# Kernel optimization log

Measured on AMD Instinct MI355X. Metric: run time of the kernel, lower is better.

## Reference

```python
import jax, jax.numpy as jnp
import numpy as np

N_NODES = 25000
N_EDGES = 400000
FEAT = 128
HID = 64
HEADS = 4
NUM_CLASSES = 2
NUM_GRAPHS = 64


def setup_inputs() -> dict:
    key = jax.random.key(0)
    ks = jax.random.split(key, 16)
    x = jax.random.normal(ks[0], (N_NODES, FEAT), dtype=jnp.float32)
    edge_index = jax.random.randint(ks[1], (2, N_EDGES), 0, N_NODES, dtype=jnp.int32)
    batch = jnp.sort(jax.random.randint(ks[2], (N_NODES,), 0, NUM_GRAPHS, dtype=jnp.int32))
    s = 1.0 / np.sqrt(FEAT)
    sh = 1.0 / np.sqrt(HID)
    shc = 1.0 / np.sqrt(HID * HEADS)
    return {
        "x": x,
        "edge_index": edge_index,
        "batch": batch,
        # conv1: GraphConv(FEAT -> HID): lin_rel (bias) on aggregated neighbors + lin_root (no bias)
        "W1_rel": jax.random.uniform(ks[3], (FEAT, HID), jnp.float32, -s, s),
        "b1": jnp.zeros((HID,), jnp.float32),
        "W1_root": jax.random.uniform(ks[4], (FEAT, HID), jnp.float32, -s, s),
        # conv3: GATConv(HID -> HID, heads=HEADS), concat output [N, HEADS*HID]
        "Wg": jax.random.uniform(ks[5], (HID, HEADS * HID), jnp.float32, -sh, sh),
        "att_src": jax.random.uniform(ks[6], (HEADS, HID), jnp.float32, -sh, sh),
        "att_dst": jax.random.uniform(ks[7], (HEADS, HID), jnp.float32, -sh, sh),
        "bg": jnp.zeros((HEADS * HID,), jnp.float32),
        # conv5: GraphConv(HEADS*HID -> HID)
        "W5_rel": jax.random.uniform(ks[8], (HEADS * HID, HID), jnp.float32, -shc, shc),
        "b5": jnp.zeros((HID,), jnp.float32),
        "W5_root": jax.random.uniform(ks[9], (HEADS * HID, HID), jnp.float32, -shc, shc),
        # fc head
        "W_fc1": jax.random.uniform(ks[10], (HID, HID), jnp.float32, -sh, sh),
        "b_fc1": jnp.zeros((HID,), jnp.float32),
        "W_fc2": jax.random.uniform(ks[11], (HID, NUM_CLASSES), jnp.float32, -sh, sh),
        "b_fc2": jnp.zeros((NUM_CLASSES,), jnp.float32),
    }


def _graph_conv(h, src, dst, W_rel, b, W_root):
    # PyG GraphConv (aggr='add'): out_i = W_rel @ sum_{j->i} h_j + b + W_root @ h_i
    agg = jax.ops.segment_sum(h[src], dst, num_segments=N_NODES)
    return agg @ W_rel + b + h @ W_root


def _gat_conv(h, src, dst, Wg, att_src, att_dst, bg):
    # GATConv with default add_self_loops=True; eval mode (no attn dropout)
    n = h.shape[0]
    loop = jnp.arange(n, dtype=src.dtype)
    si = jnp.concatenate([src, loop])
    di = jnp.concatenate([dst, loop])
    xl = (h @ Wg).reshape(n, HEADS, HID)              # [N, H, C]
    a_s = jnp.sum(xl * att_src, axis=-1)              # [N, H]
    a_d = jnp.sum(xl * att_dst, axis=-1)              # [N, H]
    e = jax.nn.leaky_relu(a_s[si] + a_d[di], 0.2)     # [E', H]
    m = jax.ops.segment_max(e, di, num_segments=n)
    p = jnp.exp(e - m[di])
    denom = jax.ops.segment_sum(p, di, num_segments=n)
    alpha = p / denom[di]                             # segment softmax over incoming edges
    out = jax.ops.segment_sum(alpha[:, :, None] * xl[si], di, num_segments=n)
    return out.reshape(n, HEADS * HID) + bg


def reference(x, edge_index, batch, W1_rel, b1, W1_root, Wg, att_src, att_dst, bg,
              W5_rel, b5, W5_root, W_fc1, b_fc1, W_fc2, b_fc2):
    src, dst = edge_index[0], edge_index[1]
    h = jax.nn.relu(_graph_conv(x, src, dst, W1_rel, b1, W1_root))
    h = jax.nn.relu(_gat_conv(h, src, dst, Wg, att_src, att_dst, bg))
    h = jax.nn.relu(_graph_conv(h, src, dst, W5_rel, b5, W5_root))
    g = jax.ops.segment_sum(h, batch, num_segments=NUM_GRAPHS)   # global_add_pool
    g = jax.nn.relu(g @ W_fc1 + b_fc1)
    return jax.nn.sigmoid(g @ W_fc2 + b_fc2)
```

## Files before the change

### kernel.cpp

```cpp
#include <hip/hip_runtime.h>
#include <math.h>

#define N_NODES 25000
#define N_EDGES 400000
#define FEAT 128
#define HID 64
#define HEADS 4
#define HH 256
#define NUM_GRAPHS 64
#define BUCKET 96
#define HS 1601536
#define NPH 25600
#define FILL_BLOCKS 1563

typedef unsigned short ushort_t;
typedef unsigned int uint_t;
typedef __attribute__((ext_vector_type(8))) short short8;
typedef __attribute__((ext_vector_type(4))) float f32x4;

__device__ __forceinline__ float lrelu(float x){ return x > 0.f ? x : 0.2f*x; }

__device__ __forceinline__ ushort_t f2bf(float f){
  uint_t u = __float_as_uint(f);
  return (ushort_t)((u + 0x7fffu + ((u >> 16) & 1u)) >> 16);
}
#define BF_LO(u) __uint_as_float((u) << 16)
#define BF_HI(u) __uint_as_float((u) & 0xffff0000u)

__global__ __launch_bounds__(256) void k_init(
    const float* __restrict__ W1_rel, const float* __restrict__ W1_root,
    const float* __restrict__ W5_rel, const float* __restrict__ W5_root,
    const float* __restrict__ Wg,
    ushort_t* __restrict__ wc1b, ushort_t* __restrict__ wc5b,
    ushort_t* __restrict__ wgb, float* __restrict__ g ,
    ushort_t* __restrict__ slot)
{
  const int e = blockIdx.x*256 + threadIdx.x;
  {
    int j=e&7, lane=(e>>3)&63, kc=(e>>9)&3, nt=e>>11;
    int k = kc*32 + (lane>>4)*8 + j, n = nt*16 + (lane&15);
    float v = (n < 64) ? W1_rel[k*64 + n] : W1_root[k*64 + n - 64];
    wc1b[e] = f2bf(v);
  }
  {
    int j=e&7, lane=(e>>3)&63, kt=(e>>9)&1, nt=e>>10;
    int k = kt*32 + (lane>>4)*8 + j, n = nt*16 + (lane&15);
    wgb[e] = f2bf(Wg[k*HH + n]);
  }
  #pragma unroll
  for (int e5 = e; e5 < 32768; e5 += 16384){
    int j=e5&7, lane=(e5>>3)&63, kc=(e5>>9)&7, nt=e5>>12;
    int k = kc*32 + (lane>>4)*8 + j, n = nt*16 + (lane&15);
    float v = (n < 64) ? W5_rel[k*64 + n] : W5_root[k*64 + n - 64];
    wc5b[e5] = f2bf(v);
  }
  int* z = (int*)g;
  for (int i = e; i < 4096 + N_NODES; i += 16384) z[i] = 0;
  const uint4 zz = {0,0,0,0};
  for (int n = e; n < N_NODES; n += 16384){
    uint4* p = (uint4*)(slot + (size_t)n*BUCKET);
    p[0] = zz; p[1] = zz; p[2] = zz; p[3] = zz;
  }
}

__global__ __launch_bounds__(256) void k_c1_fill(
    const int* __restrict__ src, const int* __restrict__ dst,
    int* __restrict__ cnt, ushort_t* __restrict__ slot,
    const float* __restrict__ X, const ushort_t* __restrict__ wc1b,
    const float* __restrict__ bias,
    ushort_t* __restrict__ out_rel_b, ushort_t* __restrict__ out_root_b)
{
  if (blockIdx.x < FILL_BLOCKS){
    const int e = blockIdx.x*256 + threadIdx.x;
    if (e < N_EDGES){
      int d = dst[e];
      int pos = atomicAdd(&cnt[d], 1);
      if (pos < BUCKET) slot[(size_t)d*BUCKET + pos] = (ushort_t)src[e];
    }
    return;
  }
  const int wid  = __builtin_amdgcn_readfirstlane(threadIdx.x >> 6);
  const int lane = threadIdx.x & 63;
  const int quad = lane >> 4, col = lane & 15;
  const int nb = (blockIdx.x - FILL_BLOCKS)*64 + wid*16;
  if (nb >= N_NODES) return;
  const int row = min(nb + col, N_NODES-1);
  const float* __restrict__ xr = X + (size_t)row*FEAT + quad*8;
  short8 a[4];
  #pragma unroll
  for (int kc = 0; kc < 4; kc++){
    #pragma unroll
    for (int j = 0; j < 8; j++)
      ((ushort_t*)&a[kc])[j] = f2bf(xr[kc*32 + j]);
  }
  #pragma unroll
  for (int nt = 0; nt < 8; nt++){
    f32x4 d = {0.f,0.f,0.f,0.f};
    #pragma unroll
    for (int kc = 0; kc < 4; kc++){
      short8 b = *(const short8*)(wc1b + ((size_t)(nt*4+kc)*64 + lane)*8);
      d = __builtin_amdgcn_mfma_f32_16x16x32_bf16(a[kc], b, d, 0, 0, 0);
    }
    if (nt < 4){
      #pragma unroll
      for (int r = 0; r < 4; r++){
        const int node = nb + quad*4 + r;
        if (node < N_NODES)
          out_rel_b[(size_t)node*HID + nt*16 + col] = f2bf(d[r]);
      }
    } else {
      const float bv = bias[(nt-4)*16 + col];
      #pragma unroll
      for (int r = 0; r < 4; r++){
        const int node = nb + quad*4 + r;
        if (node < N_NODES)
          out_root_b[(size_t)node*HID + (nt-4)*16 + col] = f2bf(d[r] + bv);
      }
    }
  }
}

__global__ __launch_bounds__(256) void conv5_mfma(
    const ushort_t* __restrict__ h2b_hm, const ushort_t* __restrict__ wc5b,
    const float* __restrict__ bias,
    ushort_t* __restrict__ out_rel_b, ushort_t* __restrict__ out_root_b)
{
  const int wid  = __builtin_amdgcn_readfirstlane(threadIdx.x >> 6);
  const int lane = threadIdx.x & 63;
  const int quad = lane >> 4, col = lane & 15;
  const int nb = blockIdx.x*64 + wid*16;
  if (nb >= N_NODES) return;
  const int row = nb + col;
  short8 a[8];
  #pragma unroll
  for (int kc = 0; kc < 8; kc++){
    const int k0 = kc*32 + quad*8;
    a[kc] = *(const short8*)(h2b_hm + (size_t)(k0>>6)*HS
                             + (size_t)row*HID + (k0&63));
  }
  #pragma unroll
  for (int nt = 0; nt < 8; nt++){
    f32x4 d = {0.f,0.f,0.f,0.f};
    #pragma unroll
    for (int kc = 0; kc < 8; kc++){
      short8 b = *(const short8*)(wc5b + ((size_t)(nt*8+kc)*64 + lane)*8);
      d = __builtin_amdgcn_mfma_f32_16x16x32_bf16(a[kc], b, d, 0, 0, 0);
    }
    if (nt < 4){
      #pragma unroll
      for (int r = 0; r < 4; r++){
        const int node = nb + quad*4 + r;
        if (node < N_NODES)
          out_rel_b[(size_t)node*HID + nt*16 + col] = f2bf(d[r]);
      }
    } else {
      const float bv = bias[(nt-4)*16 + col];
      #pragma unroll
      for (int r = 0; r < 4; r++){
        const int node = nb + quad*4 + r;
        if (node < N_NODES)
          out_root_b[(size_t)node*HID + (nt-4)*16 + col] = f2bf(d[r] + bv);
      }
    }
  }
}

__global__ __launch_bounds__(256) void k3_mfma(
    const ushort_t* __restrict__ h1b, const ushort_t* __restrict__ wgb,
    const float* __restrict__ att_src, const float* __restrict__ att_dst,
    ushort_t* __restrict__ xlb_hm, float* __restrict__ a_s_hm,
    float* __restrict__ a_d_hm)
{
  const int wid  = __builtin_amdgcn_readfirstlane(threadIdx.x >> 6);
  const int lane = threadIdx.x & 63;
  const int quad = lane >> 4, col = lane & 15;
  const int nb = blockIdx.x*64 + wid*16;
  const ushort_t* arow = h1b + (size_t)(nb + col)*HID + quad*8;
  short8 a0 = *(const short8*)(arow);
  short8 a1 = *(const short8*)(arow + 32);
  float as_acc[4] = {0,0,0,0}, ad_acc[4] = {0,0,0,0};
  #pragma unroll
  for (int nt = 0; nt < 16; nt++){
    short8 b0 = *(const short8*)(wgb + ((size_t)(nt*2+0)*64 + lane)*8);
    short8 b1 = *(const short8*)(wgb + ((size_t)(nt*2+1)*64 + lane)*8);
    f32x4 d = {0.f, 0.f, 0.f, 0.f};
    d = __builtin_amdgcn_mfma_f32_16x16x32_bf16(a0, b0, d, 0, 0, 0);
    d = __builtin_amdgcn_mfma_f32_16x16x32_bf16(a1, b1, d, 0, 0, 0);
    const int h = nt >> 2;
    const float asv = att_src[h*HID + (nt & 3)*16 + col];
    const float adv = att_dst[h*HID + (nt & 3)*16 + col];
    #pragma unroll
    for (int r = 0; r < 4; r++){
      const int node = nb + quad*4 + r;
      if (node < N_NODES)
        xlb_hm[(size_t)h*HS + (size_t)node*HID + (nt&3)*16 + col] = f2bf(d[r]);
      as_acc[r] += d[r]*asv;
      ad_acc[r] += d[r]*adv;
    }
    if ((nt & 3) == 3){
      #pragma unroll
      for (int r = 0; r < 4; r++){
        float s1 = as_acc[r], s2 = ad_acc[r];
        #pragma unroll
        for (int off = 1; off < 16; off <<= 1){
          s1 += __shfl_xor(s1, off, 64);
          s2 += __shfl_xor(s2, off, 64);
        }
        const int node = nb + quad*4 + r;
        if (col == 0 && node < N_NODES){
          a_s_hm[h*NPH + node] = s1;
          a_d_hm[h*NPH + node] = s2;
        }
        as_acc[r] = 0.f; ad_acc[r] = 0.f;
      }
    }
  }
}

template<int MODE>
__global__ __launch_bounds__(256, 8) void k_aggb(
    const int* __restrict__ cnt, const ushort_t* __restrict__ slot,
    const ushort_t* __restrict__ featb, const ushort_t* __restrict__ rootb,
    const int* __restrict__ batch, float* __restrict__ g,
    ushort_t* __restrict__ outb)
{
  __shared__ float red[3*HID];
  const int node = blockIdx.x;
  const int w    = threadIdx.x >> 6;
  const int lane = threadIdx.x & 63;
  const ushort_t* __restrict__ sl = slot + (size_t)node*BUCKET;
  const int4 pk = ((const int4*)sl)[w];
  uint_t rt = 0;
  if (w == 0) rt = rootb[(size_t)node*HID + lane];
  const int deg = min(cnt[node], BUCKET);
  const uint_t pw[4] = {(uint_t)pk.x, (uint_t)pk.y, (uint_t)pk.z, (uint_t)pk.w};
  uint_t u[8];
  #pragma unroll
  for (int j = 0; j < 8; j++){
    const uint_t s = (j & 1) ? (pw[j>>1] >> 16) : (pw[j>>1] & 0xffffu);
    u[j] = featb[(size_t)s*HID + lane];
  }
  float acc = 0.f;
  #pragma unroll
  for (int j = 0; j < 8; j++)
    acc += (w*8 + j < deg) ? BF_LO(u[j]) : 0.f;
  if (w == 3)
    for (int t = 32; t < deg; t++)
      acc += BF_LO((uint_t)featb[(size_t)sl[t]*HID + lane]);
  if (w) red[(w-1)*HID + lane] = acc;
  __syncthreads();
  if (w == 0){
    acc += red[lane] + red[HID + lane] + red[2*HID + lane];
    acc += BF_LO(rt);
    const float v = fmaxf(acc, 0.f);
    if (MODE == 0){
      outb[(size_t)node*HID + lane] = f2bf(v);
    } else {
      const int b = batch[node];
      atomicAdd(&g[b*HID + lane], v);
    }
  }
}

__global__ __launch_bounds__(256) void k_gat_node(
    const int* __restrict__ cnt, const ushort_t* __restrict__ slot,
    const ushort_t* __restrict__ xlb_hm, const float* __restrict__ a_s_hm,
    const float* __restrict__ a_d_hm, const float* __restrict__ bg,
    ushort_t* __restrict__ h2b_hm)
{
  const int head = blockIdx.x & 3;
  const int node = (blockIdx.x >> 2)*16 + (threadIdx.x >> 4);
  if (node >= N_NODES) return;
  const int lane = threadIdx.x & 63;
  const int cl = lane & 15;
  const int gb = lane & 48;
  const ushort_t* __restrict__ sl = slot + (size_t)node*BUCKET;
  const int deg = min(cnt[node], BUCKET);
  const ushort_t* __restrict__ xlh = xlb_hm + (size_t)head*HS;
  const float* __restrict__ ash = a_s_hm + head*NPH;
  const float adh = a_d_hm[head*NPH + node];
  float acc0=0, acc1=0, acc2=0, acc3=0;
  float dsum = 0.f;
  for (int base = 0; base < deg; base += 16){
    float pme = 0.f; int sme = node;
    const int e = base + cl;
    if (e < deg){
      sme = sl[e];
      pme = __expf(lrelu(ash[sme] + adh));
    }
    dsum += pme;
    const int nsub = min(16, deg - base);
    int s = 0;
    for (; s + 2 <= nsub; s += 2){
      const float pA = __shfl(pme, gb + s, 64);
      const int   sA = __shfl(sme, gb + s, 64);
      const float pB = __shfl(pme, gb + s + 1, 64);
      const int   sB = __shfl(sme, gb + s + 1, 64);
      uint2 rA = ((const uint2*)(xlh + (size_t)sA*HID))[cl];
      uint2 rB = ((const uint2*)(xlh + (size_t)sB*HID))[cl];
      acc0 += pA*BF_LO(rA.x); acc1 += pA*BF_HI(rA.x);
      acc2 += pA*BF_LO(rA.y); acc3 += pA*BF_HI(rA.y);
      acc0 += pB*BF_LO(rB.x); acc1 += pB*BF_HI(rB.x);
      acc2 += pB*BF_LO(rB.y); acc3 += pB*BF_HI(rB.y);
    }
    if (s < nsub){
      const float pA = __shfl(pme, gb + s, 64);
      const int   sA = __shfl(sme, gb + s, 64);
      uint2 rA = ((const uint2*)(xlh + (size_t)sA*HID))[cl];
      acc0 += pA*BF_LO(rA.x); acc1 += pA*BF_HI(rA.x);
      acc2 += pA*BF_LO(rA.y); acc3 += pA*BF_HI(rA.y);
    }
  }
  #pragma unroll
  for (int off = 1; off < 16; off <<= 1) dsum += __shfl_xor(dsum, off, 64);
  const float pself = __expf(lrelu(ash[node] + adh));
  const float inv = 1.f / (dsum + pself);
  uint2 r = ((const uint2*)(xlh + (size_t)node*HID))[cl];
  acc0 += pself*BF_LO(r.x); acc1 += pself*BF_HI(r.x);
  acc2 += pself*BF_LO(r.y); acc3 += pself*BF_HI(r.y);
  const int col0 = head*HID + cl*4;
  const float ox = fmaxf(acc0*inv + bg[col0+0], 0.f);
  const float oy = fmaxf(acc1*inv + bg[col0+1], 0.f);
  const float oz = fmaxf(acc2*inv + bg[col0+2], 0.f);
  const float ow = fmaxf(acc3*inv + bg[col0+3], 0.f);
  uint2 o;
  o.x = (uint_t)f2bf(ox) | ((uint_t)f2bf(oy) << 16);
  o.y = (uint_t)f2bf(oz) | ((uint_t)f2bf(ow) << 16);
  ((uint2*)(h2b_hm + (size_t)head*HS + (size_t)node*HID))[cl] = o;
}

__global__ __launch_bounds__(256) void k_head(
    const float* __restrict__ g, const float* __restrict__ W1,
    const float* __restrict__ b1, const float* __restrict__ W2,
    const float* __restrict__ b2, float* __restrict__ out)
{
  __shared__ float gs[NUM_GRAPHS*HID];
  __shared__ float hh[NUM_GRAPHS*HID];
  for (int i = threadIdx.x; i < NUM_GRAPHS*HID; i += 256) gs[i] = g[i];
  __syncthreads();
  for (int t = threadIdx.x; t < NUM_GRAPHS*HID; t += 256){
    int b = t >> 6, j = t & 63;
    float acc = b1[j];
    for (int k = 0; k < HID; k++) acc += gs[b*HID+k]*W1[k*HID+j];
    hh[t] = fmaxf(acc, 0.f);
  }
  __syncthreads();
  for (int t = threadIdx.x; t < NUM_GRAPHS*2; t += 256){
    int b = t >> 1, c = t & 1;
    float acc = b2[c];
    for (int k = 0; k < HID; k++) acc += hh[b*HID+k]*W2[k*2+c];
    out[t] = 1.f / (1.f + __expf(-acc));
  }
}

extern "C" void kernel_launch(void* const* d_in, const int* in_sizes, int n_in,
                              void* d_out, int out_size, void* d_ws, size_t ws_size,
                              hipStream_t stream)
{
  const float* x       = (const float*)d_in[0];
  const int*   ei      = (const int*)d_in[1];
  const int*   batch   = (const int*)d_in[2];
  const float* W1_rel  = (const float*)d_in[3];
  const float* b1      = (const float*)d_in[4];
  const float* W1_root = (const float*)d_in[5];
  const float* Wg      = (const float*)d_in[6];
  const float* att_src = (const float*)d_in[7];
  const float* att_dst = (const float*)d_in[8];
  const float* bg      = (const float*)d_in[9];
  const float* W5_rel  = (const float*)d_in[10];
  const float* b5      = (const float*)d_in[11];
  const float* W5_root = (const float*)d_in[12];
  const float* W_fc1   = (const float*)d_in[13];
  const float* b_fc1   = (const float*)d_in[14];
  const float* W_fc2   = (const float*)d_in[15];
  const float* b_fc2   = (const float*)d_in[16];
  const int* src = ei;
  const int* dst = ei + N_EDGES;

  float* ws    = (float*)d_ws;
  ushort_t* xr_b   = (ushort_t*)ws;
  ushort_t* rootb  = (ushort_t*)(ws + 800800);
  ushort_t* h1b    = (ushort_t*)(ws + 2402400);
  ushort_t* xlb_hm = (ushort_t*)(ws + 3203200);
  float*    a_s_hm = ws + 6406304;
  float*    a_d_hm = ws + 6508704;
  ushort_t* h2b_hm = (ushort_t*)(ws + 6611104);
  float*    g      = ws + 9814200;
  int*      cnt    = (int*)(ws + 9818296);
  ushort_t* wc1b   = (ushort_t*)(ws + 9843296);
  ushort_t* wc5b   = (ushort_t*)(ws + 9851488);
  ushort_t* wgb    = (ushort_t*)(ws + 9867872);
  ushort_t* slot   = (ushort_t*)(ws + 9876064);
  float*    out    = (float*)d_out;

  k_init<<<64,256,0,stream>>>(W1_rel, W1_root, W5_rel, W5_root, Wg,
                              wc1b, wc5b, wgb, g, slot);

  k_c1_fill<<<FILL_BLOCKS + (N_NODES+63)/64,256,0,stream>>>(
      src, dst, cnt, slot, x, wc1b, b1, xr_b, rootb);

  k_aggb<0><<<N_NODES,256,0,stream>>>(cnt, slot, xr_b, rootb, nullptr, nullptr, h1b);

  k3_mfma<<<(N_NODES+63)/64,256,0,stream>>>(h1b, wgb, att_src, att_dst,
                                            xlb_hm, a_s_hm, a_d_hm);
  k_gat_node<<<((N_NODES+15)/16)*HEADS,256,0,stream>>>(cnt, slot,
      xlb_hm, a_s_hm, a_d_hm, bg, h2b_hm);

  conv5_mfma<<<(N_NODES+63)/64,256,0,stream>>>(h2b_hm, wc5b, b5, xr_b, rootb);
  k_aggb<1><<<N_NODES,256,0,stream>>>(cnt, slot, xr_b, rootb, batch, g, nullptr);

  k_head<<<1,256,0,stream>>>(g, W_fc1, b_fc1, W_fc2, b_fc2, out);
}
```

Before: 260.1 us.

## Fuse conv1 neighbor aggregation into GAT projection MFMA kernel via LDS

Replaces the separate conv1 aggregation kernel and the GAT linear/attention MFMA kernel with one kernel. Each wave gathers neighbor features for its 16 nodes, two nodes at a time with software-pipelined loads, and writes the ReLU'd bf16 rows to shared memory. It then feeds them directly into the MFMA projection. This removes a launch and the h1 round trip through global memory. In exchange, per-node gather parallelism drops from 256 threads per node to a 64-lane wave handling nodes serially, with heavy register use for the prefetched data, which may lower occupancy and latency hiding.

```diff
diff --git a/kernel.cpp b/kernel.cpp
--- a/kernel.cpp
+++ b/kernel.cpp
@@ -165,19 +165,94 @@
   }
 }
 
-__global__ __launch_bounds__(256) void k3_mfma(
-    const ushort_t* __restrict__ h1b, const ushort_t* __restrict__ wgb,
+__device__ __forceinline__ void agg_ldslot(
+    const int* __restrict__ cnt, const ushort_t* __restrict__ slot,
+    const ushort_t* __restrict__ rootb, int nv, int lane,
+    uint_t pw[16], int &deg, uint_t &rt)
+{
+  const ushort_t* __restrict__ sl = slot + (size_t)nv*BUCKET;
+  const int4 A = ((const int4*)sl)[0];
+  const int4 B = ((const int4*)sl)[1];
+  const int4 C = ((const int4*)sl)[2];
+  const int4 D = ((const int4*)sl)[3];
+  pw[0]=(uint_t)A.x; pw[1]=(uint_t)A.y; pw[2]=(uint_t)A.z; pw[3]=(uint_t)A.w;
+  pw[4]=(uint_t)B.x; pw[5]=(uint_t)B.y; pw[6]=(uint_t)B.z; pw[7]=(uint_t)B.w;
+  pw[8]=(uint_t)C.x; pw[9]=(uint_t)C.y; pw[10]=(uint_t)C.z; pw[11]=(uint_t)C.w;
+  pw[12]=(uint_t)D.x; pw[13]=(uint_t)D.y; pw[14]=(uint_t)D.z; pw[15]=(uint_t)D.w;
+  deg = min(cnt[nv], BUCKET);
+  rt  = rootb[(size_t)nv*HID + lane];
+}
+__device__ __forceinline__ void agg_gather(
+    const ushort_t* __restrict__ featb, const uint_t pw[16], int lane,
+    uint_t u[32])
+{
+  #pragma unroll
+  for (int j = 0; j < 32; j++){
+    const uint_t s = (j & 1) ? (pw[j>>1] >> 16) : (pw[j>>1] & 0xffffu);
+    u[j] = featb[(size_t)s*HID + lane];
+  }
+}
+__device__ __forceinline__ float agg_acc(const uint_t u[32], int deg, uint_t rt)
+{
+  float acc = BF_LO(rt);
+  #pragma unroll
+  for (int j = 0; j < 32; j++)
+    acc += (j < deg) ? BF_LO(u[j]) : 0.f;
+  return acc;
+}
+
+__global__ __launch_bounds__(256) void k_agg3(
+    const int* __restrict__ cnt, const ushort_t* __restrict__ slot,
+    const ushort_t* __restrict__ featb, const ushort_t* __restrict__ rootb,
+    const ushort_t* __restrict__ wgb,
     const float* __restrict__ att_src, const float* __restrict__ att_dst,
     ushort_t* __restrict__ xlb_hm, float* __restrict__ a_s_hm,
     float* __restrict__ a_d_hm)
 {
+  __shared__ ushort_t h1s[64][80];
   const int wid  = __builtin_amdgcn_readfirstlane(threadIdx.x >> 6);
   const int lane = threadIdx.x & 63;
+  const int nb = blockIdx.x*64;
+  const int rbase = wid*16;
+  const int nb0 = nb + rbase;
+
+  {
+    uint_t pwA[16], pwB[16], uA[32], uB[32], rtA, rtB;
+    int degA, degB;
+    agg_ldslot(cnt, slot, rootb, min(nb0+0, N_NODES-1), lane, pwA, degA, rtA);
+    agg_ldslot(cnt, slot, rootb, min(nb0+1, N_NODES-1), lane, pwB, degB, rtB);
+    agg_gather(featb, pwA, lane, uA);
+    agg_gather(featb, pwB, lane, uB);
+    for (int k = 0; k < 8; k++){
+      float aA = agg_acc(uA, degA, rtA);
+      float aB = agg_acc(uB, degB, rtB);
+      if (degA > 32){
+        const ushort_t* sl = slot + (size_t)min(nb0+2*k,   N_NODES-1)*BUCKET;
+        for (int t = 32; t < degA; t++)
+          aA += BF_LO((uint_t)featb[(size_t)sl[t]*HID + lane]);
+      }
+      if (degB > 32){
+        const ushort_t* sl = slot + (size_t)min(nb0+2*k+1, N_NODES-1)*BUCKET;
+        for (int t = 32; t < degB; t++)
+          aB += BF_LO((uint_t)featb[(size_t)sl[t]*HID + lane]);
+      }
+      h1s[rbase + 2*k    ][lane] = f2bf(fmaxf(aA, 0.f));
+      h1s[rbase + 2*k + 1][lane] = f2bf(fmaxf(aB, 0.f));
+      if (k < 7){
+        agg_ldslot(cnt, slot, rootb, min(nb0+2*k+2, N_NODES-1), lane,
+                   pwA, degA, rtA);
+        agg_ldslot(cnt, slot, rootb, min(nb0+2*k+3, N_NODES-1), lane,
+                   pwB, degB, rtB);
+        agg_gather(featb, pwA, lane, uA);
+        agg_gather(featb, pwB, lane, uB);
+      }
+    }
+  }
+  __syncthreads();
+
   const int quad = lane >> 4, col = lane & 15;
-  const int nb = blockIdx.x*64 + wid*16;
-  const ushort_t* arow = h1b + (size_t)(nb + col)*HID + quad*8;
-  short8 a0 = *(const short8*)(arow);
-  short8 a1 = *(const short8*)(arow + 32);
+  short8 a0 = *(const short8*)&h1s[rbase + col][quad*8];
+  short8 a1 = *(const short8*)&h1s[rbase + col][quad*8 + 32];
   float as_acc[4] = {0,0,0,0}, ad_acc[4] = {0,0,0,0};
   #pragma unroll
   for (int nt = 0; nt < 16; nt++){
@@ -191,7 +266,7 @@
     const float adv = att_dst[h*HID + (nt & 3)*16 + col];
     #pragma unroll
     for (int r = 0; r < 4; r++){
-      const int node = nb + quad*4 + r;
+      const int node = nb0 + quad*4 + r;
       if (node < N_NODES)
         xlb_hm[(size_t)h*HS + (size_t)node*HID + (nt&3)*16 + col] = f2bf(d[r]);
       as_acc[r] += d[r]*asv;
@@ -206,7 +281,7 @@
           s1 += __shfl_xor(s1, off, 64);
           s2 += __shfl_xor(s2, off, 64);
         }
-        const int node = nb + quad*4 + r;
+        const int node = nb0 + quad*4 + r;
         if (col == 0 && node < N_NODES){
           a_s_hm[h*NPH + node] = s1;
           a_d_hm[h*NPH + node] = s2;
@@ -217,12 +292,10 @@
   }
 }
 
-template<int MODE>
 __global__ __launch_bounds__(256, 8) void k_aggb(
     const int* __restrict__ cnt, const ushort_t* __restrict__ slot,
     const ushort_t* __restrict__ featb, const ushort_t* __restrict__ rootb,
-    const int* __restrict__ batch, float* __restrict__ g,
-    ushort_t* __restrict__ outb)
+    const int* __restrict__ batch, float* __restrict__ g)
 {
   __shared__ float red[3*HID];
   const int node = blockIdx.x;
@@ -253,12 +326,8 @@
     acc += red[lane] + red[HID + lane] + red[2*HID + lane];
     acc += BF_LO(rt);
     const float v = fmaxf(acc, 0.f);
-    if (MODE == 0){
-      outb[(size_t)node*HID + lane] = f2bf(v);
-    } else {
-      const int b = batch[node];
-      atomicAdd(&g[b*HID + lane], v);
-    }
+    const int b = batch[node];
+    atomicAdd(&g[b*HID + lane], v);
   }
 }
 
@@ -380,7 +449,6 @@
   float* ws    = (float*)d_ws;
   ushort_t* xr_b   = (ushort_t*)ws;
   ushort_t* rootb  = (ushort_t*)(ws + 800800);
-  ushort_t* h1b    = (ushort_t*)(ws + 2402400);
   ushort_t* xlb_hm = (ushort_t*)(ws + 3203200);
   float*    a_s_hm = ws + 6406304;
   float*    a_d_hm = ws + 6508704;
@@ -399,15 +467,14 @@
   k_c1_fill<<<FILL_BLOCKS + (N_NODES+63)/64,256,0,stream>>>(
       src, dst, cnt, slot, x, wc1b, b1, xr_b, rootb);
 
-  k_aggb<0><<<N_NODES,256,0,stream>>>(cnt, slot, xr_b, rootb, nullptr, nullptr, h1b);
-
-  k3_mfma<<<(N_NODES+63)/64,256,0,stream>>>(h1b, wgb, att_src, att_dst,
-                                            xlb_hm, a_s_hm, a_d_hm);
+  k_agg3<<<(N_NODES+63)/64,256,0,stream>>>(cnt, slot, xr_b, rootb, wgb,
+      att_src, att_dst, xlb_hm, a_s_hm, a_d_hm);
+
   k_gat_node<<<((N_NODES+15)/16)*HEADS,256,0,stream>>>(cnt, slot,
       xlb_hm, a_s_hm, a_d_hm, bg, h2b_hm);
 
   conv5_mfma<<<(N_NODES+63)/64,256,0,stream>>>(h2b_hm, wc5b, b5, xr_b, rootb);
-  k_aggb<1><<<N_NODES,256,0,stream>>>(cnt, slot, xr_b, rootb, batch, g, nullptr);
+  k_aggb<<<N_NODES,256,0,stream>>>(cnt, slot, xr_b, rootb, batch, g);
 
   k_head<<<1,256,0,stream>>>(g, W_fc1, b_fc1, W_fc2, b_fc2, out);
 }
```

Result: no change. 259.0 us (-0.4%).
